# Kernel tuning notes

Hardware: AMD Instinct MI355X
Metric: run time of the kernel (lower is better)

The kernel has to match this reference:

```python
import jax, jax.numpy as jnp
import numpy as np
import math

B, T, C, H = 2, 2048, 1024, 16
HD = C // H
WINDOW = 256  # local_attn_ctx with attnblocksize=1


def setup_inputs() -> dict:
    key = jax.random.key(0)
    k1, k2, k3 = jax.random.split(key, 3)
    x = jax.random.normal(k1, (B, T, C), dtype=jnp.float32)
    Wqkv = jax.random.normal(k2, (C, 3 * C), dtype=jnp.float32) * 0.02
    bqkv = jnp.zeros((3 * C,), dtype=jnp.float32)
    Wproj = jax.random.normal(k3, (C, C), dtype=jnp.float32) * 0.02
    bproj = jnp.zeros((C,), dtype=jnp.float32)
    # 'local' block-sparse layout at token granularity: causal + sliding window
    i = np.arange(T)[:, None]
    j = np.arange(T)[None, :]
    mask = ((j <= i) & (i - j <= WINDOW)).astype(np.int32)
    return {"x": x, "Wqkv": Wqkv, "bqkv": bqkv, "Wproj": Wproj, "bproj": bproj,
            "mask": jnp.asarray(mask)}


def reference(x, Wqkv, bqkv, Wproj, bproj, mask):
    Bb, Tt, Cc = x.shape
    qkv = (x @ Wqkv + bqkv).reshape(Bb, Tt, 3, H, HD)  # [B,T,3,H,hd]
    q = jnp.transpose(qkv[:, :, 0], (0, 2, 1, 3))  # [B,H,T,hd]
    k = jnp.transpose(qkv[:, :, 1], (0, 2, 1, 3))
    v = jnp.transpose(qkv[:, :, 2], (0, 2, 1, 3))
    scale = 1.0 / math.sqrt(HD)
    att = jnp.einsum('bhqd,bhkd->bhqk', q, k) * scale  # dense T x T scores
    att = jnp.where(mask[:Tt, :Tt] == 0, -jnp.inf, att)
    att = jax.nn.softmax(att, axis=-1)
    y = jnp.einsum('bhqk,bhkd->bhqd', att, v)
    y = jnp.transpose(y, (0, 2, 1, 3)).reshape(Bb, Tt, Cc)
    return y @ Wproj + bproj
```

## Files before the change

### kernel.cpp

```cpp
#include <hip/hip_runtime.h>
#include <hip/hip_bf16.h>
#include <math.h>

typedef __bf16 bf16;
typedef __attribute__((ext_vector_type(8))) __bf16 bf16x8;
typedef __attribute__((ext_vector_type(4))) __bf16 bf16x4;
typedef __attribute__((ext_vector_type(4))) float f32x4;

#define B_  2
#define T_  2048
#define C_  1024
#define H_  16
#define HD_ 64
#define WIN_ 256

#define GLOAD16(g, l)                                                        \
  __builtin_amdgcn_global_load_lds(                                          \
      (const __attribute__((address_space(1))) void*)(g),                    \
      (__attribute__((address_space(3))) void*)(l), 16, 0, 0)

__device__ inline void bar() {
  asm volatile("" ::: "memory");
  __builtin_amdgcn_s_barrier();
  asm volatile("" ::: "memory");
}


__global__ __launch_bounds__(256) void cvt_f32_bf16_k(const float* __restrict__ in,
                                                      bf16* __restrict__ out) {
  int idx = blockIdx.x * 256 + threadIdx.x;
  const float4 v = ((const float4*)in)[idx];
  bf16x4 o;
  o[0] = (bf16)v.x; o[1] = (bf16)v.y; o[2] = (bf16)v.z; o[3] = (bf16)v.w;
  ((bf16x4*)out)[idx] = o;
}

__global__ __launch_bounds__(256) void transpose_cvt_k(const float* __restrict__ W,
                                                       bf16* __restrict__ WT,
                                                       int K, int N) {
  __shared__ float t[32][33];
  int n0 = blockIdx.x * 32, k0 = blockIdx.y * 32;
  int tx = threadIdx.x, ty = threadIdx.y;
  #pragma unroll
  for (int i = 0; i < 32; i += 8)
    t[ty + i][tx] = W[(size_t)(k0 + ty + i) * N + (n0 + tx)];
  __syncthreads();
  #pragma unroll
  for (int i = 0; i < 32; i += 8)
    WT[(size_t)(n0 + ty + i) * K + (k0 + tx)] = (bf16)t[tx][ty + i];
}


template <int TM, int TN, int WM, int WN, int MINW, int MODE>
__global__ __launch_bounds__(WM * WN * 64, MINW)
void gemm_db_k(const bf16* __restrict__ A, const bf16* __restrict__ Bt,
               const float* __restrict__ bias,
               void* __restrict__ out0, void* __restrict__ out1,
               int M, int N, int K) {
  constexpr int NW    = WM * WN;
  constexpr int WROWS = TM / WM;
  constexpr int WCOLS = TN / WN;
  constexpr int FM    = WROWS / 16;
  constexpr int FN    = WCOLS / 16;
  constexpr int NCH   = (TM + TN) / 8;
  constexpr int CPW   = NCH / NW;

  const int bm = blockIdx.x * TM;
  const int bn = blockIdx.y * TN;
  const int tid  = threadIdx.x;
  const int wid  = tid >> 6;
  const int lane = tid & 63;
  const int wr = wid / WN;
  const int wc = wid % WN;
  const int lr = lane & 15;
  const int g  = lane >> 4;

  __shared__ bf16 As[2][TM * 64];
  __shared__ bf16 Bs[2][TN * 64];

  f32x4 acc[FM][FN] = {};

  const int sr = lane >> 3;
  const int sc = ((lane & 7) ^ sr) << 3;

  #define STG(p_, u_)                                                        \
    do {                                                                     \
      _Pragma("unroll")                                                      \
      for (int i = 0; i < CPW; ++i) {                                        \
        const int c = wid * CPW + i;                                         \
        if (c < TM / 8) {                                                    \
          GLOAD16(A + (size_t)(bm + c * 8 + sr) * K + (u_) * 64 + sc,        \
                  &As[p_][c * 8 * 64]);                                      \
        } else {                                                             \
          GLOAD16(Bt + (size_t)(bn + (c - TM / 8) * 8 + sr) * K + (u_) * 64 + sc, \
                  &Bs[p_][(c - TM / 8) * 8 * 64]);                           \
        }                                                                    \
      }                                                                      \
    } while (0)

  const int NT = K >> 6;
  const int kc0 = ((0 + g) ^ (lr & 7)) << 3;
  const int kc1 = ((4 + g) ^ (lr & 7)) << 3;

  STG(0, 0);
  asm volatile("s_waitcnt vmcnt(0)" ::: "memory");
  __builtin_amdgcn_s_barrier();
  asm volatile("" ::: "memory");

  for (int u = 0; u < NT; ++u) {
    const int p = u & 1;
    if (u + 1 < NT) {
      STG(p ^ 1, u + 1);
      asm volatile("s_waitcnt vmcnt(%0)" :: "i"(CPW) : "memory");
    } else {
      asm volatile("s_waitcnt vmcnt(0)" ::: "memory");
    }
    bar();

    const bf16* Ar = &As[p][(wr * WROWS + lr) * 64];
    const bf16* Br = &Bs[p][(wc * WCOLS + lr) * 64];
    #pragma unroll
    for (int s = 0; s < 2; ++s) {
      const int kc = s ? kc1 : kc0;
      bf16x8 av[FM], bvv[FN];
      #pragma unroll
      for (int m = 0; m < FM; ++m)
        av[m] = *(const bf16x8*)(Ar + m * 16 * 64 + kc);
      #pragma unroll
      for (int n = 0; n < FN; ++n)
        bvv[n] = *(const bf16x8*)(Br + n * 16 * 64 + kc);
      __builtin_amdgcn_s_setprio(1);
      #pragma unroll
      for (int m = 0; m < FM; ++m)
        #pragma unroll
        for (int n = 0; n < FN; ++n)
          acc[m][n] = __builtin_amdgcn_mfma_f32_16x16x32_bf16(av[m], bvv[n], acc[m][n], 0, 0, 0);
      __builtin_amdgcn_s_setprio(0);
    }
    bar();
  }
  #undef STG

  const int orow = g * 4;
  #pragma unroll
  for (int n = 0; n < FN; ++n) {
    const int nbase = bn + wc * WCOLS + n * 16;
    const int gn = nbase + lr;
    const float bv_ = bias[gn];
    #pragma unroll
    for (int m = 0; m < FM; ++m) {
      const int gm0 = bm + wr * WROWS + m * 16 + orow;
      if (MODE == 0) {
        #pragma unroll
        for (int r = 0; r < 4; ++r)
          ((float*)out0)[(size_t)(gm0 + r) * N + gn] = acc[m][n][r] + bv_;
      } else {
        if (nbase < 2 * C_) {
          #pragma unroll
          for (int r = 0; r < 4; ++r)
            ((bf16*)out0)[(size_t)(gm0 + r) * (2 * C_) + gn] = (bf16)(acc[m][n][r] + bv_);
        } else {
          const int vcol = gn - 2 * C_;
          const int h = vcol >> 6, d = vcol & 63;
          const int b = gm0 >> 11, tok = gm0 & (T_ - 1);
          bf16x4 o;
          #pragma unroll
          for (int r = 0; r < 4; ++r) o[r] = (bf16)(acc[m][n][r] + bv_);
          *(bf16x4*)&((bf16*)out1)[(((size_t)b * H_ + h) * HD_ + d) * T_ + tok] = o;
        }
      }
    }
  }
}


__global__ __launch_bounds__(256) void attn_mfma_k(const bf16* __restrict__ qk,
                                                   const bf16* __restrict__ vt,
                                                   bf16* __restrict__ y) {
  const int q0 = blockIdx.x * 64;
  const int h  = blockIdx.y;
  const int b  = blockIdx.z;
  const int tid  = threadIdx.x;
  const int wid  = tid >> 6;
  const int lane = tid & 63;
  const int lr = lane & 15;
  const int g  = lane >> 4;

  __shared__ bf16 Ks[64][72];
  __shared__ bf16 Vs[64][72];
  __shared__ bf16 Ps[4][16][72];

  const int qrow = q0 + wid * 16 + lr;
  const bf16* qptr = qk + ((size_t)(b * T_ + qrow)) * (2 * C_) + h * HD_;
  bf16x8 qf[2];
  qf[0] = *(const bf16x8*)(qptr + g * 8);
  qf[1] = *(const bf16x8*)(qptr + 32 + g * 8);

  float m = -1e30f, l = 0.f;
  f32x4 yacc[4] = {};

  const int kt_lo = (blockIdx.x >= 4) ? (int)blockIdx.x - 4 : 0;
  for (int kt = kt_lo; kt <= (int)blockIdx.x; ++kt) {
    __syncthreads();
    #pragma unroll
    for (int i = 0; i < 2; ++i) {
      int cc = tid + i * 256;
      int rr = cc >> 3;
      int c0 = (cc & 7) * 8;
      *(bf16x8*)&Ks[rr][c0] = *(const bf16x8*)&qk[((size_t)(b * T_) + kt * 64 + rr) * (2 * C_) + C_ + h * HD_ + c0];
      *(bf16x8*)&Vs[rr][c0] = *(const bf16x8*)&vt[(((size_t)b * H_ + h) * HD_ + rr) * T_ + kt * 64 + c0];
    }
    __syncthreads();

    f32x4 sacc[4] = {};
    #pragma unroll
    for (int t = 0; t < 4; ++t)
      #pragma unroll
      for (int s = 0; s < 2; ++s)
        sacc[t] = __builtin_amdgcn_mfma_f32_16x16x32_bf16(
            *(const bf16x8*)&Ks[t * 16 + lr][s * 32 + g * 8], qf[s], sacc[t], 0, 0, 0);

    float pv[4][4];
    float rmax = -1e30f;
    #pragma unroll
    for (int t = 0; t < 4; ++t)
      #pragma unroll
      for (int r = 0; r < 4; ++r) {
        const int key = kt * 64 + t * 16 + g * 4 + r;
        const bool valid = (key <= qrow) && (qrow - key <= WIN_);
        const float sv = valid ? sacc[t][r] * 0.125f : -__builtin_inff();
        pv[t][r] = sv;
        rmax = fmaxf(rmax, sv);
      }
    rmax = fmaxf(rmax, __shfl_xor(rmax, 16));
    rmax = fmaxf(rmax, __shfl_xor(rmax, 32));

    const float mnew = fmaxf(m, rmax);
    const float alpha = __expf(m - mnew);
    m = mnew;
    float lsum = 0.f;
    #pragma unroll
    for (int t = 0; t < 4; ++t)
      #pragma unroll
      for (int r = 0; r < 4; ++r) {
        const float e = __expf(pv[t][r] - mnew);
        pv[t][r] = e;
        lsum += e;
      }
    lsum += __shfl_xor(lsum, 16);
    lsum += __shfl_xor(lsum, 32);
    l = l * alpha + lsum;

    #pragma unroll
    for (int t = 0; t < 4; ++t) {
      bf16x4 pk;
      #pragma unroll
      for (int r = 0; r < 4; ++r) pk[r] = (bf16)pv[t][r];
      *(bf16x4*)&Ps[wid][lr][t * 16 + g * 4] = pk;
    }

    float al[4];
    #pragma unroll
    for (int r = 0; r < 4; ++r) al[r] = __shfl(alpha, g * 4 + r);
    #pragma unroll
    for (int t = 0; t < 4; ++t)
      #pragma unroll
      for (int r = 0; r < 4; ++r) yacc[t][r] *= al[r];

    bf16x8 pf[2];
    pf[0] = *(const bf16x8*)&Ps[wid][lr][g * 8];
    pf[1] = *(const bf16x8*)&Ps[wid][lr][32 + g * 8];
    #pragma unroll
    for (int t = 0; t < 4; ++t)
      #pragma unroll
      for (int s = 0; s < 2; ++s)
        yacc[t] = __builtin_amdgcn_mfma_f32_16x16x32_bf16(
            pf[s], *(const bf16x8*)&Vs[t * 16 + lr][s * 32 + g * 8], yacc[t], 0, 0, 0);
  }

  float li[4];
  #pragma unroll
  for (int r = 0; r < 4; ++r) li[r] = 1.f / __shfl(l, g * 4 + r);
  #pragma unroll
  for (int t = 0; t < 4; ++t)
    #pragma unroll
    for (int r = 0; r < 4; ++r) {
      const int tok = q0 + wid * 16 + g * 4 + r;
      y[((size_t)(b * T_ + tok)) * C_ + h * HD_ + t * 16 + lr] = (bf16)(yacc[t][r] * li[r]);
    }
}


extern "C" void kernel_launch(void* const* d_in, const int* in_sizes, int n_in,
                              void* d_out, int out_size, void* d_ws, size_t ws_size,
                              hipStream_t stream) {
  const float* x     = (const float*)d_in[0];
  const float* Wqkv  = (const float*)d_in[1];
  const float* bqkv  = (const float*)d_in[2];
  const float* Wproj = (const float*)d_in[3];
  const float* bproj = (const float*)d_in[4];
  float* out = (float*)d_out;

  const size_t SZ_QK  = (size_t)B_ * T_ * 2 * C_ * sizeof(bf16);
  const size_t SZ_VT  = (size_t)B_ * H_ * HD_ * T_ * sizeof(bf16);
  const size_t SZ_XB  = (size_t)B_ * T_ * C_ * sizeof(bf16);
  const size_t SZ_WQT = (size_t)3 * C_ * C_ * sizeof(bf16);
  const size_t SZ_WPT = (size_t)C_ * C_ * sizeof(bf16);
  const size_t NEED   = SZ_QK + SZ_VT + SZ_XB + SZ_WQT + SZ_WPT + SZ_XB;
  if (ws_size < NEED) return;

  char* ws = (char*)d_ws;
  bf16* qkb    = (bf16*)(ws);
  bf16* vtb    = (bf16*)(ws + SZ_QK);
  bf16* xb     = (bf16*)(ws + SZ_QK + SZ_VT);
  bf16* wqkvT  = (bf16*)(ws + SZ_QK + SZ_VT + SZ_XB);
  bf16* wprojT = (bf16*)(ws + SZ_QK + SZ_VT + SZ_XB + SZ_WQT);
  bf16* yb     = (bf16*)(ws + SZ_QK + SZ_VT + SZ_XB + SZ_WQT + SZ_WPT);

  cvt_f32_bf16_k<<<4096, 256, 0, stream>>>(x, xb);
  transpose_cvt_k<<<dim3(3 * C_ / 32, C_ / 32), dim3(32, 8), 0, stream>>>(Wqkv, wqkvT, C_, 3 * C_);
  transpose_cvt_k<<<dim3(C_ / 32, C_ / 32), dim3(32, 8), 0, stream>>>(Wproj, wprojT, C_, C_);

  gemm_db_k<128, 192, 2, 4, 4, 2><<<dim3((B_ * T_) / 128, (3 * C_) / 192), 512, 0, stream>>>(
      xb, wqkvT, bqkv, qkb, vtb, B_ * T_, 3 * C_, C_);

  attn_mfma_k<<<dim3(T_ / 64, H_, B_), 256, 0, stream>>>(qkb, vtb, yb);

  gemm_db_k<64, 128, 2, 2, 2, 0><<<dim3((B_ * T_) / 64, C_ / 128), 256, 0, stream>>>(
      yb, wprojT, bproj, out, nullptr, B_ * T_, C_, C_);
}
```

Measured before the change: 84.92 us.

## Double-buffer K/V tiles with register prefetch in local attention kernel

```diff
diff --git a/kernel.cpp b/kernel.cpp
--- a/kernel.cpp
+++ b/kernel.cpp
@@ -186,8 +186,8 @@
   const int lr = lane & 15;
   const int g  = lane >> 4;
 
-  __shared__ bf16 Ks[64][72];
-  __shared__ bf16 Vs[64][72];
+  __shared__ bf16 Ks[2][64][72];
+  __shared__ bf16 Vs[2][64][72];
   __shared__ bf16 Ps[4][16][72];
 
   const int qrow = q0 + wid * 16 + lr;
@@ -200,25 +200,41 @@
   f32x4 yacc[4] = {};
 
   const int kt_lo = (blockIdx.x >= 4) ? (int)blockIdx.x - 4 : 0;
-  for (int kt = kt_lo; kt <= (int)blockIdx.x; ++kt) {
-    __syncthreads();
-    #pragma unroll
-    for (int i = 0; i < 2; ++i) {
-      int cc = tid + i * 256;
-      int rr = cc >> 3;
-      int c0 = (cc & 7) * 8;
-      *(bf16x8*)&Ks[rr][c0] = *(const bf16x8*)&qk[((size_t)(b * T_) + kt * 64 + rr) * (2 * C_) + C_ + h * HD_ + c0];
-      *(bf16x8*)&Vs[rr][c0] = *(const bf16x8*)&vt[(((size_t)b * H_ + h) * HD_ + rr) * T_ + kt * 64 + c0];
-    }
-    __syncthreads();
+  const int kt_hi = blockIdx.x;
+
+  const int rr0 = tid >> 3, rr1 = (tid + 256) >> 3;
+  const int c00 = (tid & 7) * 8, c01 = ((tid + 256) & 7) * 8;
+
+  #define LOADKV(kt_)                                                          \
+    do {                                                                       \
+      const size_t kb = ((size_t)(b * T_) + (kt_) * 64);                       \
+      kreg0 = *(const bf16x8*)&qk[(kb + rr0) * (2 * C_) + C_ + h * HD_ + c00]; \
+      kreg1 = *(const bf16x8*)&qk[(kb + rr1) * (2 * C_) + C_ + h * HD_ + c01]; \
+      vreg0 = *(const bf16x8*)&vt[(((size_t)b * H_ + h) * HD_ + rr0) * T_ + (kt_) * 64 + c00]; \
+      vreg1 = *(const bf16x8*)&vt[(((size_t)b * H_ + h) * HD_ + rr1) * T_ + (kt_) * 64 + c01]; \
+    } while (0)
+
+  bf16x8 kreg0, kreg1, vreg0, vreg1;
+  LOADKV(kt_lo);
+
+  for (int kt = kt_lo; kt <= kt_hi; ++kt) {
+    const int p = kt & 1;
+    *(bf16x8*)&Ks[p][rr0][c00] = kreg0;
+    *(bf16x8*)&Ks[p][rr1][c01] = kreg1;
+    *(bf16x8*)&Vs[p][rr0][c00] = vreg0;
+    *(bf16x8*)&Vs[p][rr1][c01] = vreg1;
+    bar();
+    if (kt + 1 <= kt_hi) LOADKV(kt + 1);
 
     f32x4 sacc[4] = {};
+    __builtin_amdgcn_s_setprio(1);
     #pragma unroll
     for (int t = 0; t < 4; ++t)
       #pragma unroll
       for (int s = 0; s < 2; ++s)
         sacc[t] = __builtin_amdgcn_mfma_f32_16x16x32_bf16(
-            *(const bf16x8*)&Ks[t * 16 + lr][s * 32 + g * 8], qf[s], sacc[t], 0, 0, 0);
+            *(const bf16x8*)&Ks[p][t * 16 + lr][s * 32 + g * 8], qf[s], sacc[t], 0, 0, 0);
+    __builtin_amdgcn_s_setprio(0);
 
     float pv[4][4];
     float rmax = -1e30f;
@@ -270,13 +286,16 @@
     bf16x8 pf[2];
     pf[0] = *(const bf16x8*)&Ps[wid][lr][g * 8];
     pf[1] = *(const bf16x8*)&Ps[wid][lr][32 + g * 8];
+    __builtin_amdgcn_s_setprio(1);
     #pragma unroll
     for (int t = 0; t < 4; ++t)
       #pragma unroll
       for (int s = 0; s < 2; ++s)
         yacc[t] = __builtin_amdgcn_mfma_f32_16x16x32_bf16(
-            pf[s], *(const bf16x8*)&Vs[t * 16 + lr][s * 32 + g * 8], yacc[t], 0, 0, 0);
+            pf[s], *(const bf16x8*)&Vs[p][t * 16 + lr][s * 32 + g * 8], yacc[t], 0, 0, 0);
+    __builtin_amdgcn_s_setprio(0);
   }
+  #undef LOADKV
 
   float li[4];
   #pragma unroll
```

Measured after the change: 87.09 us. 2.6% more time.
